# Kernel optimization log

Hardware: AMD Instinct MI355X
Metric: run time of the kernel (lower is better)

## Reference

```python
import jax, jax.numpy as jnp
import numpy as np

N_NODES = 50000
N_EDGES = 800000
IN_CH = 64
HID = 128
EPS = 1e-12  # F.normalize default eps


def setup_inputs() -> dict:
    key = jax.random.key(0)
    ks = jax.random.split(key, 12)
    x = jax.random.normal(ks[0], (N_NODES, IN_CH), dtype=jnp.float32)
    edge_index = jax.random.randint(ks[1], (2, N_EDGES), 0, N_NODES, dtype=jnp.int64)
    def lin(k, out_c, in_c):
        bound = 1.0 / np.sqrt(in_c)
        return jax.random.uniform(k, (out_c, in_c), jnp.float32, -bound, bound)
    # layer 0: in->hid ; layers 1,2: hid->hid
    Wl0 = lin(ks[2], HID, IN_CH); bl0 = jnp.zeros((HID,), jnp.float32); Wr0 = lin(ks[3], HID, IN_CH)
    Wl1 = lin(ks[4], HID, HID);  bl1 = jnp.zeros((HID,), jnp.float32); Wr1 = lin(ks[5], HID, HID)
    Wl2 = lin(ks[6], HID, HID);  bl2 = jnp.zeros((HID,), jnp.float32); Wr2 = lin(ks[7], HID, HID)
    return {"x": x, "edge_index": edge_index,
            "Wl0": Wl0, "bl0": bl0, "Wr0": Wr0,
            "Wl1": Wl1, "bl1": bl1, "Wr1": Wr1,
            "Wl2": Wl2, "bl2": bl2, "Wr2": Wr2}


def _sage_conv(h, src, dst, Wl, bl, Wr, n_nodes):
    # mean aggregation of source-node features at target nodes
    msg = h[src]                                                   # [E, d]
    agg = jax.ops.segment_sum(msg, dst, num_segments=n_nodes)      # [N, d]
    cnt = jax.ops.segment_sum(jnp.ones((src.shape[0],), h.dtype), dst,
                              num_segments=n_nodes)                # [N]
    mean = agg / jnp.maximum(cnt, 1.0)[:, None]
    out = mean @ Wl.T + bl + h @ Wr.T                              # lin_l(agg)+lin_r(x)
    # L2 normalize (F.normalize, p=2)
    norm = jnp.maximum(jnp.linalg.norm(out, axis=-1, keepdims=True), EPS)
    return out / norm


def reference(x, edge_index, Wl0, bl0, Wr0, Wl1, bl1, Wr1, Wl2, bl2, Wr2):
    src, dst = edge_index[0], edge_index[1]
    n = x.shape[0]
    h = _sage_conv(x, src, dst, Wl0, bl0, Wr0, n)
    h = jax.nn.relu(h)  # dropout is identity in eval mode
    h = _sage_conv(h, src, dst, Wl1, bl1, Wr1, n)
    h = jax.nn.relu(h)
    h = _sage_conv(h, src, dst, Wl2, bl2, Wr2, n)
    return h
```

## Files before the change

kernel.cpp:

```cpp
#include <hip/hip_runtime.h>

#define NN 50000
#define NNP 50016
#define NE 800000
#define DIN 64
#define HD 128
#define NBUK 196
#define SB 196
#define BCAP 12288

typedef __attribute__((ext_vector_type(8))) short short8;
typedef __attribute__((ext_vector_type(4))) float f32x4;
typedef __attribute__((ext_vector_type(4))) unsigned short us4;
typedef __attribute__((ext_vector_type(8))) unsigned short us8;

__device__ __forceinline__ unsigned short f2bf(float f) {
    unsigned int u = __float_as_uint(f);
    u = (u + 0x7FFFu + ((u >> 16) & 1u)) >> 16;
    return (unsigned short)u;
}
__device__ __forceinline__ float bf2f(unsigned short u) {
    return __uint_as_float(((unsigned int)u) << 16);
}

#define LDS_SCAN256(a, t)                                 \
    for (int off_ = 1; off_ < 256; off_ <<= 1) {          \
        int add_ = ((t) >= off_) ? (a)[(t) - off_] : 0;   \
        __syncthreads();                                  \
        (a)[t] += add_;                                   \
        __syncthreads();                                  \
    }


__global__ void zero_meta(int* __restrict__ meta) {
    meta[threadIdx.x] = 0;
}

__global__ __launch_bounds__(256) void bucket_count(const int* __restrict__ dst,
                                                    int* __restrict__ bcnt) {
    __shared__ int lc[256];
    int t = threadIdx.x;
    lc[t] = 0;
    __syncthreads();
    int base = blockIdx.x * 4096 + t * 16;
#pragma unroll
    for (int j = 0; j < 4; ++j) {
        int e = base + j * 4;
        if (e < NE) {
            int4 d = *(const int4*)(dst + e);
            atomicAdd(&lc[d.x >> 8], 1);
            atomicAdd(&lc[d.y >> 8], 1);
            atomicAdd(&lc[d.z >> 8], 1);
            atomicAdd(&lc[d.w >> 8], 1);
        }
    }
    __syncthreads();
    if (t < NBUK && lc[t] > 0) atomicAdd(&bcnt[t], lc[t]);
}

__global__ __launch_bounds__(256) void bucket_scan(const int* __restrict__ bcnt,
                                                   int* __restrict__ bbase,
                                                   int* __restrict__ rowptr) {
    __shared__ int sh[256];
    int t = threadIdx.x;
    int v = (t < NBUK) ? bcnt[t] : 0;
    sh[t] = v;
    __syncthreads();
    LDS_SCAN256(sh, t);
    if (t < NBUK) bbase[t] = sh[t] - v;
    if (t == NBUK - 1) bbase[NBUK] = sh[t];
    if (t == 0) rowptr[NN] = NE;
}

__global__ __launch_bounds__(256) void bucket_scatter(
    const int* __restrict__ src, const int* __restrict__ dst,
    const int* __restrict__ bbase, int* __restrict__ bfill,
    int2* __restrict__ pairs) {
    __shared__ int cnt[256];
    __shared__ int incl[256];
    __shared__ int lfill[256];
    __shared__ int rung[256];
    __shared__ int2 buf[4096];
    int t = threadIdx.x;
    cnt[t] = 0;
    lfill[t] = 0;
    __syncthreads();
    int base = blockIdx.x * 4096 + t * 16;
#pragma unroll
    for (int j = 0; j < 4; ++j) {
        int e = base + j * 4;
        if (e < NE) {
            int4 d = *(const int4*)(dst + e);
            atomicAdd(&cnt[d.x >> 8], 1);
            atomicAdd(&cnt[d.y >> 8], 1);
            atomicAdd(&cnt[d.z >> 8], 1);
            atomicAdd(&cnt[d.w >> 8], 1);
        }
    }
    __syncthreads();
    incl[t] = cnt[t];
    __syncthreads();
    LDS_SCAN256(incl, t);
    int c = cnt[t];
    if (t < NBUK && c > 0) rung[t] = bbase[t] + atomicAdd(&bfill[t], c);
    __syncthreads();
#pragma unroll
    for (int j = 0; j < 4; ++j) {
        int e = base + j * 4;
        if (e < NE) {
            int4 s4 = *(const int4*)(src + e);
            int4 d4 = *(const int4*)(dst + e);
            int ss[4] = {s4.x, s4.y, s4.z, s4.w};
            int dd[4] = {d4.x, d4.y, d4.z, d4.w};
#pragma unroll
            for (int q = 0; q < 4; ++q) {
                int k = dd[q] >> 8;
                int p = (incl[k] - cnt[k]) + atomicAdd(&lfill[k], 1);
                buf[p] = {ss[q], dd[q]};
            }
        }
    }
    __syncthreads();
    int n = min(4096, NE - blockIdx.x * 4096);
    for (int i = t; i < n; i += 256) {
        int2 pr = buf[i];
        int k = pr.y >> 8;
        pairs[rung[k] + (i - (incl[k] - cnt[k]))] = pr;
    }
}

__global__ __launch_bounds__(256) void build_csr(
    const int2* __restrict__ pairs, const int* __restrict__ bbase,
    int* __restrict__ rowptr, float* __restrict__ invcnt,
    int* __restrict__ csr_src) {
    __shared__ int cnt[256];
    __shared__ int incl[256];
    __shared__ int lfill[256];
    __shared__ int sbuf[BCAP];
    int b = blockIdx.x, t = threadIdx.x;
    int pbeg = bbase[b], pend = bbase[b + 1];
    int sz = pend - pbeg;
    cnt[t] = 0;
    lfill[t] = 0;
    __syncthreads();
    for (int i = t; i < sz; i += 256)
        atomicAdd(&cnt[pairs[pbeg + i].y & 255], 1);
    __syncthreads();
    incl[t] = cnt[t];
    __syncthreads();
    LDS_SCAN256(incl, t);
    int node = b * 256 + t;
    int c = cnt[t];
    if (node < NN) {
        rowptr[node] = pbeg + incl[t] - c;
        invcnt[node] = 1.0f / (float)(c > 0 ? c : 1);
    }
    if (sz <= BCAP) {
        for (int i = t; i < sz; i += 256) {
            int2 pr = pairs[pbeg + i];
            int ld = pr.y & 255;
            sbuf[(incl[ld] - cnt[ld]) + atomicAdd(&lfill[ld], 1)] = pr.x;
        }
        __syncthreads();
        for (int i = t; i < sz; i += 256) csr_src[pbeg + i] = sbuf[i];
    } else {
        for (int i = t; i < sz; i += 256) {
            int2 pr = pairs[pbeg + i];
            int ld = pr.y & 255;
            csr_src[pbeg + (incl[ld] - cnt[ld]) + atomicAdd(&lfill[ld], 1)] = pr.x;
        }
    }
}


__device__ __forceinline__ void pack_one(const float* Wl, const float* Wr, int D,
                                         unsigned short* Wpk, int i) {
    int j = i & 7;
    int lane = (i >> 3) & 63;
    int ct = (i >> 9) & 7;
    int ks = i >> 12;
    int k = ks * 32 + ((lane >> 4) << 3) + j;
    int c = ct * 16 + (lane & 15);
    float v = (k < D) ? Wl[c * D + k] : Wr[c * D + (k - D)];
    Wpk[i] = f2bf(v);
}

__global__ void pack_weights(const float* __restrict__ Wl0, const float* __restrict__ Wr0,
                             const float* __restrict__ Wl1, const float* __restrict__ Wr1,
                             const float* __restrict__ Wl2, const float* __restrict__ Wr2,
                             unsigned short* __restrict__ Wpk0,
                             unsigned short* __restrict__ Wpk1,
                             unsigned short* __restrict__ Wpk2) {
    const int S0 = 2 * DIN * HD;
    const int S12 = 2 * HD * HD;
    int i = blockIdx.x * blockDim.x + threadIdx.x;
    if (i < S0) { pack_one(Wl0, Wr0, DIN, Wpk0, i); return; }
    int j = i - S0;
    if (j < S12) { pack_one(Wl1, Wr1, HD, Wpk1, j); return; }
    int m = j - S12;
    if (m < S12) pack_one(Wl2, Wr2, HD, Wpk2, m);
}

__global__ void conv_x(const float* __restrict__ x, unsigned short* __restrict__ A0) {
    int i = blockIdx.x * blockDim.x + threadIdx.x;
    if (i >= NN * 16) return;
    int row = i >> 4, c4 = i & 15;
    float4 v = ((const float4*)(x + (size_t)row * DIN))[c4];
    us4 o = {f2bf(v.x), f2bf(v.y), f2bf(v.z), f2bf(v.w)};
    *(us4*)(A0 + (size_t)row * 128 + 64 + c4 * 4) = o;
}


__global__ __launch_bounds__(256) void gather_mean_x(
    const int* __restrict__ rowptr, const int* __restrict__ csr_src,
    const float* __restrict__ invcnt, unsigned short* __restrict__ A0) {
    int tid = threadIdx.x;
    int n = blockIdx.x * 4 + (tid >> 6);
    int lane = tid & 63;
    int c8 = lane & 7;
    int g = lane >> 3;
    int beg = rowptr[n], end = rowptr[n + 1];
    float acc[8] = {};
    const unsigned short* hb = A0 + 64 + (size_t)c8 * 8;
    int e = beg + g;
    for (; e + 8 < end; e += 16) {
        int s0 = csr_src[e], s1 = csr_src[e + 8];
        us8 v0 = *(const us8*)(hb + (size_t)s0 * 128);
        us8 v1 = *(const us8*)(hb + (size_t)s1 * 128);
#pragma unroll
        for (int j = 0; j < 8; ++j) acc[j] += bf2f(v0[j]) + bf2f(v1[j]);
    }
    if (e < end) {
        us8 v0 = *(const us8*)(hb + (size_t)csr_src[e] * 128);
#pragma unroll
        for (int j = 0; j < 8; ++j) acc[j] += bf2f(v0[j]);
    }
#pragma unroll
    for (int j = 0; j < 8; ++j) {
        acc[j] += __shfl_xor(acc[j], 8, 64);
        acc[j] += __shfl_xor(acc[j], 16, 64);
        acc[j] += __shfl_xor(acc[j], 32, 64);
    }
    if (g == 0) {
        float ic = invcnt[n];
        us8 o;
#pragma unroll
        for (int j = 0; j < 8; ++j) o[j] = f2bf(acc[j] * ic);
        *(us8*)(A0 + (size_t)n * 128 + c8 * 8) = o;
    }
}


__global__ __launch_bounds__(256) void gather_mean_h(
    const unsigned short* __restrict__ A12, const int* __restrict__ rowptr,
    const int* __restrict__ csr_src, const float* __restrict__ invcnt,
    unsigned short* __restrict__ Am) {
    int tid = threadIdx.x;
    int n = blockIdx.x * 4 + (tid >> 6);
    int lane = tid & 63;
    int c8 = lane & 15;
    int g = lane >> 4;
    int beg = rowptr[n], end = rowptr[n + 1];
    float acc[8] = {};
    const unsigned short* hb = A12 + 128 + (size_t)c8 * 8;
    int e = beg + g;
    for (; e + 4 < end; e += 8) {
        int s0 = csr_src[e], s1 = csr_src[e + 4];
        us8 v0 = *(const us8*)(hb + (size_t)s0 * 256);
        us8 v1 = *(const us8*)(hb + (size_t)s1 * 256);
#pragma unroll
        for (int j = 0; j < 8; ++j) acc[j] += bf2f(v0[j]) + bf2f(v1[j]);
    }
    if (e < end) {
        us8 v0 = *(const us8*)(hb + (size_t)csr_src[e] * 256);
#pragma unroll
        for (int j = 0; j < 8; ++j) acc[j] += bf2f(v0[j]);
    }
#pragma unroll
    for (int j = 0; j < 8; ++j) {
        acc[j] += __shfl_xor(acc[j], 16, 64);
        acc[j] += __shfl_xor(acc[j], 32, 64);
    }
    if (g == 0) {
        float ic = invcnt[n];
        us8 o;
#pragma unroll
        for (int j = 0; j < 8; ++j) o[j] = f2bf(acc[j] * ic);
        *(us8*)(Am + (size_t)n * 256 + c8 * 8) = o;
    }
}


template <int K, bool RELU, bool F32OUT, bool BF16H>
__global__ __launch_bounds__(256) void linear_mfma(
    const unsigned short* __restrict__ A, const unsigned short* __restrict__ Wpk,
    const float* __restrict__ bias, float* __restrict__ outF,
    unsigned short* __restrict__ Hn ) {
    constexpr int NK = K / 32;
    __shared__ float rsum[2][32];
    int tid = threadIdx.x;
    int lane = tid & 63, w = tid >> 6;
    int rg = w >> 1, cg = w & 1;
    int r0 = blockIdx.x * 32 + rg * 16;
    int row_l = lane & 15, kb = lane >> 4;

    const unsigned short* Arow = A + (size_t)(r0 + row_l) * K + kb * 8;
    const unsigned short* Wp = Wpk + ((size_t)(cg * 4) * 64 + lane) * 8;

    f32x4 acc[4] = {{0.f, 0.f, 0.f, 0.f}, {0.f, 0.f, 0.f, 0.f},
                    {0.f, 0.f, 0.f, 0.f}, {0.f, 0.f, 0.f, 0.f}};
#pragma unroll
    for (int ks = 0; ks < NK; ++ks) {
        short8 a = *(const short8*)(Arow + ks * 32);
#pragma unroll
        for (int t = 0; t < 4; ++t) {
            short8 b = *(const short8*)(Wp + ((size_t)ks * 8 + t) * 64 * 8);
            acc[t] = __builtin_amdgcn_mfma_f32_16x16x32_bf16(a, b, acc[t], 0, 0, 0);
        }
    }

    float sq[4] = {0.f, 0.f, 0.f, 0.f};
#pragma unroll
    for (int t = 0; t < 4; ++t) {
        float bv = bias[cg * 64 + t * 16 + row_l];
#pragma unroll
        for (int r = 0; r < 4; ++r) {
            acc[t][r] += bv;
            sq[r] = fmaf(acc[t][r], acc[t][r], sq[r]);
        }
    }
#pragma unroll
    for (int off = 1; off < 16; off <<= 1)
#pragma unroll
        for (int r = 0; r < 4; ++r) sq[r] += __shfl_xor(sq[r], off, 64);

    if (row_l == 0) {
#pragma unroll
        for (int r = 0; r < 4; ++r) rsum[cg][rg * 16 + kb * 4 + r] = sq[r];
    }
    __syncthreads();

    int rbase = rg * 16 + kb * 4;
#pragma unroll
    for (int r = 0; r < 4; ++r) {
        int row = r0 + kb * 4 + r;
        if (row >= NN) continue;
        float n2 = rsum[0][rbase + r] + rsum[1][rbase + r];
        float inv = 1.0f / fmaxf(sqrtf(n2), 1e-12f);
#pragma unroll
        for (int t = 0; t < 4; ++t) {
            float v = acc[t][r] * inv;
            if (RELU) v = fmaxf(v, 0.f);
            int c = cg * 64 + t * 16 + row_l;
            if (F32OUT) outF[(size_t)row * HD + c] = v;
            if (BF16H) Hn[(size_t)row * 256 + c] = f2bf(v);
        }
    }
}


static inline size_t align256(size_t x) { return (x + 255) & ~(size_t)255; }

extern "C" void kernel_launch(void* const* d_in, const int* in_sizes, int n_in,
                              void* d_out, int out_size, void* d_ws, size_t ws_size,
                              hipStream_t stream) {
    const float* x   = (const float*)d_in[0];
    const int*   ei  = (const int*)d_in[1];
    const float* Wl0 = (const float*)d_in[2];
    const float* bl0 = (const float*)d_in[3];
    const float* Wr0 = (const float*)d_in[4];
    const float* Wl1 = (const float*)d_in[5];
    const float* bl1 = (const float*)d_in[6];
    const float* Wr1 = (const float*)d_in[7];
    const float* Wl2 = (const float*)d_in[8];
    const float* bl2 = (const float*)d_in[9];
    const float* Wr2 = (const float*)d_in[10];

    const int* src = ei;
    const int* dst = ei + NE;

    char* p = (char*)d_ws;
    size_t off = 0;
    int* meta = (int*)(p + off);            off = align256(off + 512 * 4);
    int* bbase = (int*)(p + off);           off = align256(off + 256 * 4);
    int* rowptr = (int*)(p + off);          off = align256(off + (size_t)(NN + 1) * 4);
    int* csr_src = (int*)(p + off);         off = align256(off + (size_t)NE * 4);
    float* invcnt = (float*)(p + off);      off = align256(off + (size_t)NN * 4);
    int2* pairs = (int2*)(p + off);         off = align256(off + (size_t)NE * 8);
    unsigned short* A0 = (unsigned short*)(p + off);   off = align256(off + (size_t)NNP * 128 * 2);
    unsigned short* A12 = (unsigned short*)(p + off);  off = align256(off + (size_t)NNP * 256 * 2);
    unsigned short* Wpk0 = (unsigned short*)(p + off); off = align256(off + (size_t)2 * DIN * HD * 2);
    unsigned short* Wpk1 = (unsigned short*)(p + off); off = align256(off + (size_t)2 * HD * HD * 2);
    unsigned short* Wpk2 = (unsigned short*)(p + off); off = align256(off + (size_t)2 * HD * HD * 2);
    (void)ws_size; (void)n_in; (void)in_sizes; (void)out_size;

    int* bcnt = meta;
    int* bfill = meta + 256;
    float* out = (float*)d_out;

    zero_meta<<<1, 512, 0, stream>>>(meta);
    bucket_count<<<SB, 256, 0, stream>>>(dst, bcnt);
    bucket_scan<<<1, 256, 0, stream>>>(bcnt, bbase, rowptr);
    bucket_scatter<<<SB, 256, 0, stream>>>(src, dst, bbase, bfill, pairs);
    build_csr<<<NBUK, 256, 0, stream>>>(pairs, bbase, rowptr, invcnt, csr_src);

    const int WTOT = 2 * DIN * HD + 2 * 2 * HD * HD;
    pack_weights<<<(WTOT + 255) / 256, 256, 0, stream>>>(Wl0, Wr0, Wl1, Wr1, Wl2, Wr2,
                                                         Wpk0, Wpk1, Wpk2);
    conv_x<<<(NN * 16 + 255) / 256, 256, 0, stream>>>(x, A0);

    const int LG = NNP / 32;
    const int GG = NN / 4;

    gather_mean_x<<<GG, 256, 0, stream>>>(rowptr, csr_src, invcnt, A0);
    linear_mfma<2 * DIN, true, false, true><<<LG, 256, 0, stream>>>(
        A0, Wpk0, bl0, nullptr, A12 + 128);

    gather_mean_h<<<GG, 256, 0, stream>>>(A12, rowptr, csr_src, invcnt, A12);
    linear_mfma<2 * HD, true, false, true><<<LG, 256, 0, stream>>>(
        A12, Wpk1, bl1, nullptr, A12 + 128);

    gather_mean_h<<<GG, 256, 0, stream>>>(A12, rowptr, csr_src, invcnt, A12);
    linear_mfma<2 * HD, false, true, false><<<LG, 256, 0, stream>>>(
        A12, Wpk2, bl2, out, nullptr);
}
```

Measured before the change: 176.0 us.

## Split gather kernels by feature slice across blocks with per-node edge parallelism

```diff
diff --git a/kernel.cpp b/kernel.cpp
--- a/kernel.cpp
+++ b/kernel.cpp
@@ -8,6 +8,7 @@
 #define NBUK 196
 #define SB 196
 #define BCAP 12288
+#define NCHUNK 3125
 
 typedef __attribute__((ext_vector_type(8))) short short8;
 typedef __attribute__((ext_vector_type(4))) float f32x4;
@@ -214,39 +215,33 @@
 __global__ __launch_bounds__(256) void gather_mean_x(
     const int* __restrict__ rowptr, const int* __restrict__ csr_src,
     const float* __restrict__ invcnt, unsigned short* __restrict__ A0) {
+    int s = blockIdx.x & 7;
+    int chunk = blockIdx.x >> 3;
     int tid = threadIdx.x;
-    int n = blockIdx.x * 4 + (tid >> 6);
-    int lane = tid & 63;
-    int c8 = lane & 7;
-    int g = lane >> 3;
+    int n = chunk * 16 + (tid >> 4);
+    if (n >= NN) return;
+    int eg = tid & 15;
     int beg = rowptr[n], end = rowptr[n + 1];
     float acc[8] = {};
-    const unsigned short* hb = A0 + 64 + (size_t)c8 * 8;
-    int e = beg + g;
-    for (; e + 8 < end; e += 16) {
-        int s0 = csr_src[e], s1 = csr_src[e + 8];
-        us8 v0 = *(const us8*)(hb + (size_t)s0 * 128);
-        us8 v1 = *(const us8*)(hb + (size_t)s1 * 128);
-#pragma unroll
-        for (int j = 0; j < 8; ++j) acc[j] += bf2f(v0[j]) + bf2f(v1[j]);
-    }
-    if (e < end) {
-        us8 v0 = *(const us8*)(hb + (size_t)csr_src[e] * 128);
-#pragma unroll
-        for (int j = 0; j < 8; ++j) acc[j] += bf2f(v0[j]);
+    const unsigned short* hb = A0 + 64 + (size_t)s * 8;
+    for (int e = beg + eg; e < end; e += 16) {
+        us8 v = *(const us8*)(hb + (size_t)csr_src[e] * 128);
+#pragma unroll
+        for (int j = 0; j < 8; ++j) acc[j] += bf2f(v[j]);
     }
 #pragma unroll
     for (int j = 0; j < 8; ++j) {
+        acc[j] += __shfl_xor(acc[j], 1, 64);
+        acc[j] += __shfl_xor(acc[j], 2, 64);
+        acc[j] += __shfl_xor(acc[j], 4, 64);
         acc[j] += __shfl_xor(acc[j], 8, 64);
-        acc[j] += __shfl_xor(acc[j], 16, 64);
-        acc[j] += __shfl_xor(acc[j], 32, 64);
-    }
-    if (g == 0) {
+    }
+    if (eg == 0) {
         float ic = invcnt[n];
         us8 o;
 #pragma unroll
         for (int j = 0; j < 8; ++j) o[j] = f2bf(acc[j] * ic);
-        *(us8*)(A0 + (size_t)n * 128 + c8 * 8) = o;
+        *(us8*)(A0 + (size_t)n * 128 + s * 8) = o;
     }
 }
 
@@ -255,38 +250,33 @@
     const unsigned short* __restrict__ A12, const int* __restrict__ rowptr,
     const int* __restrict__ csr_src, const float* __restrict__ invcnt,
     unsigned short* __restrict__ Am) {
+    int s = blockIdx.x & 7;
+    int chunk = blockIdx.x >> 3;
     int tid = threadIdx.x;
-    int n = blockIdx.x * 4 + (tid >> 6);
-    int lane = tid & 63;
-    int c8 = lane & 15;
-    int g = lane >> 4;
+    int n = chunk * 16 + (tid >> 4);
+    if (n >= NN) return;
+    int l16 = tid & 15;
+    int eg = l16 >> 1, cl = l16 & 1;
     int beg = rowptr[n], end = rowptr[n + 1];
     float acc[8] = {};
-    const unsigned short* hb = A12 + 128 + (size_t)c8 * 8;
-    int e = beg + g;
-    for (; e + 4 < end; e += 8) {
-        int s0 = csr_src[e], s1 = csr_src[e + 4];
-        us8 v0 = *(const us8*)(hb + (size_t)s0 * 256);
-        us8 v1 = *(const us8*)(hb + (size_t)s1 * 256);
-#pragma unroll
-        for (int j = 0; j < 8; ++j) acc[j] += bf2f(v0[j]) + bf2f(v1[j]);
-    }
-    if (e < end) {
-        us8 v0 = *(const us8*)(hb + (size_t)csr_src[e] * 256);
-#pragma unroll
-        for (int j = 0; j < 8; ++j) acc[j] += bf2f(v0[j]);
+    const unsigned short* hb = A12 + 128 + (size_t)s * 16 + (size_t)cl * 8;
+    for (int e = beg + eg; e < end; e += 8) {
+        us8 v = *(const us8*)(hb + (size_t)csr_src[e] * 256);
+#pragma unroll
+        for (int j = 0; j < 8; ++j) acc[j] += bf2f(v[j]);
     }
 #pragma unroll
     for (int j = 0; j < 8; ++j) {
-        acc[j] += __shfl_xor(acc[j], 16, 64);
-        acc[j] += __shfl_xor(acc[j], 32, 64);
-    }
-    if (g == 0) {
+        acc[j] += __shfl_xor(acc[j], 2, 64);
+        acc[j] += __shfl_xor(acc[j], 4, 64);
+        acc[j] += __shfl_xor(acc[j], 8, 64);
+    }
+    if (eg == 0) {
         float ic = invcnt[n];
         us8 o;
 #pragma unroll
         for (int j = 0; j < 8; ++j) o[j] = f2bf(acc[j] * ic);
-        *(us8*)(Am + (size_t)n * 256 + c8 * 8) = o;
+        *(us8*)(Am + (size_t)n * 256 + s * 16 + cl * 8) = o;
     }
 }
 
@@ -410,7 +400,7 @@
     conv_x<<<(NN * 16 + 255) / 256, 256, 0, stream>>>(x, A0);
 
     const int LG = NNP / 32;
-    const int GG = NN / 4;
+    const int GG = 8 * NCHUNK;
 
     gather_mean_x<<<GG, 256, 0, stream>>>(rowptr, csr_src, invcnt, A0);
     linear_mfma<2 * DIN, true, false, true><<<LG, 256, 0, stream>>>(
```

Result: slower. 294.8 us (+67.5%).
